# Kernel tuning notes

Hardware: AMD Instinct MI355X
Metric: run time of the kernel (lower is better)

The kernel has to match this reference:

```python
import jax, jax.numpy as jnp
import numpy as np


def setup_inputs() -> dict:
    key = jax.random.key(0)
    k1, k2 = jax.random.split(key)
    B, D, L = 8192, 256, 4
    x = jax.random.normal(k1, (B, D), dtype=jnp.float32)
    # nn.Linear(d,1) weights (one row per layer) with kaiming-uniform-like scale
    W = jax.random.normal(k2, (L, D), dtype=jnp.float32) * (1.0 / np.sqrt(D))
    b_lin = jnp.zeros((L,), dtype=jnp.float32)   # linear biases (scalar per layer)
    bias = jnp.zeros((L, D), dtype=jnp.float32)  # per-layer bias params (init zeros)
    return {"x": x, "W": W, "b_lin": b_lin, "bias": bias}


def reference(x, W, b_lin, bias):
    # DCN cross: x_l = x_0 (x_l^T w_i) + b_lin_i + bias_i + x_l
    # Mathematically identical to the torch outer-product form:
    #   (x_0 @ x_l^T) @ w_i + b_lin_i == x_0 * (x_l . w_i) + b_lin_i
    num_layers = W.shape[0]
    x_0 = x
    x_l = x
    for i in range(num_layers):
        s = x_l @ W[i]                                  # [B]  (x_l . w_i)
        x_l = x_0 * s[:, None] + b_lin[i] + bias[i][None, :] + x_l
    return x_l
```

## Files before the change

kernel.cpp:

```cpp
#include <hip/hip_runtime.h>


__global__ __launch_bounds__(256) void cross_kernel(
    const float* __restrict__ x,
    const float* __restrict__ W,
    const float* __restrict__ b_lin,
    const float* __restrict__ bias,
    float* __restrict__ out,
    int B, int L)
{
    const int wave = threadIdx.x >> 6;
    const int lane = threadIdx.x & 63;
    const int row  = blockIdx.x * 4 + wave;
    if (row >= B) return;

    const float4* xrow = (const float4*)(x + (size_t)row * 256);
    float4 x0 = xrow[lane];
    float4 xl = x0;

    #pragma unroll
    for (int i = 0; i < 4; ++i) {
        if (i >= L) break;
        float4 w = ((const float4*)(W + i * 256))[lane];
        float p = xl.x * w.x + xl.y * w.y + xl.z * w.z + xl.w * w.w;
        #pragma unroll
        for (int off = 32; off > 0; off >>= 1)
            p += __shfl_xor(p, off, 64);
        const float s = p;

        float4 bi = ((const float4*)(bias + i * 256))[lane];
        const float bl = b_lin[i];

        xl.x = fmaf(x0.x, s, bl + bi.x + xl.x);
        xl.y = fmaf(x0.y, s, bl + bi.y + xl.y);
        xl.z = fmaf(x0.z, s, bl + bi.z + xl.z);
        xl.w = fmaf(x0.w, s, bl + bi.w + xl.w);
    }

    ((float4*)(out + (size_t)row * 256))[lane] = xl;
}

extern "C" void kernel_launch(void* const* d_in, const int* in_sizes, int n_in,
                              void* d_out, int out_size, void* d_ws, size_t ws_size,
                              hipStream_t stream) {
    const float* x     = (const float*)d_in[0];
    const float* W     = (const float*)d_in[1];
    const float* b_lin = (const float*)d_in[2];
    const float* bias  = (const float*)d_in[3];
    float* out = (float*)d_out;

    const int L = in_sizes[2];
    const int D = in_sizes[1] / L;
    const int B = in_sizes[0] / D;

    const int rows_per_block = 4;
    const int grid = (B + rows_per_block - 1) / rows_per_block;
    cross_kernel<<<grid, 256, 0, stream>>>(x, W, b_lin, bias, out, B, L);
}
```

Baseline: 66.68 us.

## Reformulate cross layers as scalar recurrence to batch all wave reductions

Result: slower. 73.08 us (+9.6%).

```diff
diff --git a/kernel.cpp b/kernel.cpp
--- a/kernel.cpp
+++ b/kernel.cpp
@@ -1,5 +1,9 @@
 #include <hip/hip_runtime.h>
 
+
+__device__ __forceinline__ float dot4(float4 a, float4 b) {
+    return fmaf(a.x, b.x, fmaf(a.y, b.y, fmaf(a.z, b.z, a.w * b.w)));
+}
 
 __global__ __launch_bounds__(256) void cross_kernel(
     const float* __restrict__ x,
@@ -14,30 +18,74 @@
     const int row  = blockIdx.x * 4 + wave;
     if (row >= B) return;
 
+    const float4 zero4 = make_float4(0.f, 0.f, 0.f, 0.f);
+
     const float4* xrow = (const float4*)(x + (size_t)row * 256);
-    float4 x0 = xrow[lane];
-    float4 xl = x0;
+    const float4 x0 = xrow[lane];
+
+    const float4* W4 = (const float4*)W;
+    const float4* B4 = (const float4*)bias;
+
+    const float4 w0 = (L > 0) ? W4[0 * 64 + lane] : zero4;
+    const float4 w1 = (L > 1) ? W4[1 * 64 + lane] : zero4;
+    const float4 w2 = (L > 2) ? W4[2 * 64 + lane] : zero4;
+    const float4 w3 = (L > 3) ? W4[3 * 64 + lane] : zero4;
+
+    float4 d;
+    d.x = dot4(x0, w0);
+    d.y = dot4(x0, w1);
+    d.z = dot4(x0, w2);
+    d.w = dot4(x0, w3);
+
+    float4 v = zero4;
+    float4 e = zero4;
+    if (L > 0) {
+        const float bl = b_lin[0];
+        float4 c = B4[0 * 64 + lane];
+        v.x = c.x + bl; v.y = c.y + bl; v.z = c.z + bl; v.w = c.w + bl;
+    }
+    if (L > 1) {
+        e.x = dot4(v, w1);
+        const float bl = b_lin[1];
+        float4 c = B4[1 * 64 + lane];
+        v.x += c.x + bl; v.y += c.y + bl; v.z += c.z + bl; v.w += c.w + bl;
+    }
+    if (L > 2) {
+        e.y = dot4(v, w2);
+        const float bl = b_lin[2];
+        float4 c = B4[2 * 64 + lane];
+        v.x += c.x + bl; v.y += c.y + bl; v.z += c.z + bl; v.w += c.w + bl;
+    }
+    if (L > 3) {
+        e.z = dot4(v, w3);
+        const float bl = b_lin[3];
+        float4 c = B4[3 * 64 + lane];
+        v.x += c.x + bl; v.y += c.y + bl; v.z += c.z + bl; v.w += c.w + bl;
+    }
 
     #pragma unroll
-    for (int i = 0; i < 4; ++i) {
-        if (i >= L) break;
-        float4 w = ((const float4*)(W + i * 256))[lane];
-        float p = xl.x * w.x + xl.y * w.y + xl.z * w.z + xl.w * w.w;
-        #pragma unroll
-        for (int off = 32; off > 0; off >>= 1)
-            p += __shfl_xor(p, off, 64);
-        const float s = p;
-
-        float4 bi = ((const float4*)(bias + i * 256))[lane];
-        const float bl = b_lin[i];
-
-        xl.x = fmaf(x0.x, s, bl + bi.x + xl.x);
-        xl.y = fmaf(x0.y, s, bl + bi.y + xl.y);
-        xl.z = fmaf(x0.z, s, bl + bi.z + xl.z);
-        xl.w = fmaf(x0.w, s, bl + bi.w + xl.w);
+    for (int off = 32; off > 0; off >>= 1) {
+        d.x += __shfl_xor(d.x, off, 64);
+        d.y += __shfl_xor(d.y, off, 64);
+        d.z += __shfl_xor(d.z, off, 64);
+        d.w += __shfl_xor(d.w, off, 64);
+        e.x += __shfl_xor(e.x, off, 64);
+        e.y += __shfl_xor(e.y, off, 64);
+        e.z += __shfl_xor(e.z, off, 64);
     }
 
-    ((float4*)(out + (size_t)row * 256))[lane] = xl;
+    float a = 1.0f;
+    if (L > 0) a += d.x;
+    if (L > 1) a += fmaf(a, d.y, e.x);
+    if (L > 2) a += fmaf(a, d.z, e.y);
+    if (L > 3) a += fmaf(a, d.w, e.z);
+
+    float4 o;
+    o.x = fmaf(a, x0.x, v.x);
+    o.y = fmaf(a, x0.y, v.y);
+    o.z = fmaf(a, x0.z, v.z);
+    o.w = fmaf(a, x0.w, v.w);
+    ((float4*)(out + (size_t)row * 256))[lane] = o;
 }
 
 extern "C" void kernel_launch(void* const* d_in, const int* in_sizes, int n_in,
```
